# Optimization experiments

Measured on AMD Instinct MI355X. Metric: run time of the kernel, lower is better.

## Reference

```python
import jax, jax.numpy as jnp
import numpy as np

N, D, W, S = 16384, 256, 64, 8  # utterances, embed dim, attention half-window, speakers


def setup_inputs() -> dict:
    key = jax.random.key(0)
    ks = jax.random.split(key, 8)
    scale = 1.0 / np.sqrt(D)
    return {
        "x": jax.random.normal(ks[0], (N, D), jnp.float32),
        "speaker_ids": jax.random.randint(ks[1], (N,), 0, S, jnp.int32),
        "W_att": jax.random.normal(ks[2], (D, D), jnp.float32) * scale,
        "W_pred": jax.random.normal(ks[3], (D, D), jnp.float32) * scale,
        "W_suc": jax.random.normal(ks[4], (D, D), jnp.float32) * scale,
        "W_same": jax.random.normal(ks[5], (D, D), jnp.float32) * scale,
        "W_diff": jax.random.normal(ks[6], (D, D), jnp.float32) * scale,
    }


def reference(x, speaker_ids, W_att, W_pred, W_suc, W_same, W_diff):
    n = x.shape[0]
    pad = jnp.zeros((W, D), x.dtype)
    # windowed gather: for utterance i, neighbors at offsets [-W, W-1] (2W slots)
    win_idx = jnp.arange(n)[:, None] + jnp.arange(2 * W)[None, :]  # index into padded [N+2W]
    xp = jnp.concatenate([pad, x, pad], axis=0)                    # [N+2W, D]
    windows = xp[win_idx]                                          # [N, 2W, D]
    # raw_attn[i,w] = (edge_att_weights(windows[i,w])) . x[i]
    raw_attn = jnp.einsum("nwd,ed,ne->nw", windows, W_att, x)      # [N, 2W]
    attn = jax.nn.softmax(raw_attn, axis=1)
    # relation masks over the band: j = i + offset
    offs = jnp.arange(2 * W) - W                                   # [-W, W-1]
    j = jnp.arange(n)[:, None] + offs[None, :]                     # [N, 2W]
    valid = (j >= 0) & (j < n)
    jc = jnp.clip(j, 0, n - 1)
    same_spk = speaker_ids[jc] == speaker_ids[:, None]
    masks = [
        valid & (offs >= 0)[None, :],   # pred: edges to current/future within window
        valid & (offs < 0)[None, :],    # suc: edges to past within window
        valid & same_spk,               # same speaker within window
        valid & ~same_spk,              # different speaker within window
    ]
    # relation-specific GCN aggregation: h = sum_r A_r @ (x @ W_r), A_r banded
    h = jnp.zeros_like(x)
    for Wr, m in zip([W_pred, W_suc, W_same, W_diff], masks):
        support = x @ Wr                                           # [N, D]
        sp = jnp.concatenate([pad, support, pad], axis=0)[win_idx]  # [N, 2W, D]
        h = h + jnp.einsum("nw,nwd->nd", attn * m, sp)
    return jax.nn.log_softmax(h, axis=1)
```

## Files before the change

kernel.cpp:

```cpp
#include <hip/hip_runtime.h>
#include <hip/hip_bf16.h>

typedef unsigned short u16;
typedef unsigned int u32;
typedef __attribute__((ext_vector_type(8))) short short8;
typedef __attribute__((ext_vector_type(4))) float floatx4;

#define NU 16384
#define DIM 256
#define AMS 208

#define XHo 0u
#define XLo 4194304u
#define XRo 8388608u
#define YHo 12582912u
#define YLo 16777216u
#define ST0 20971520u
#define STROW 16512u
#define STMAT 4227072u
#define WH0o 33652736u
#define WL0o 33718272u
#define WRo  33783808u

__device__ __forceinline__ u16 bfh(float v) {
  return (u16)(__float_as_uint(v) >> 16);
}
__device__ __forceinline__ float bup(u16 u) {
  return __uint_as_float(((u32)u) << 16);
}
__device__ __forceinline__ u16 bfrn(float v) {
  u32 u = __float_as_uint(v);
  return (u16)((u + 0x7fffu + ((u >> 16) & 1u)) >> 16);
}

__global__ __launch_bounds__(256) void xprep(const float* __restrict__ x,
                                             u16* __restrict__ ws) {
  int idx = (blockIdx.x * 256 + threadIdx.x) * 8;
  float4 v0 = *(const float4*)(x + idx);
  float4 v1 = *(const float4*)(x + idx + 4);
  float a[8] = {v0.x, v0.y, v0.z, v0.w, v1.x, v1.y, v1.z, v1.w};
  u16 h[8], l[8], r[8];
#pragma unroll
  for (int q = 0; q < 8; ++q) {
    h[q] = bfh(a[q]);
    l[q] = bfh(a[q] - bup(h[q]));
    r[q] = bfrn(a[q]);
  }
  *(uint4*)(ws + XHo + idx) = *(const uint4*)h;
  *(uint4*)(ws + XLo + idx) = *(const uint4*)l;
  *(uint4*)(ws + XRo + idx) = *(const uint4*)r;
}

__global__ __launch_bounds__(256) void wpgz(
    const float* __restrict__ wat, const float* __restrict__ wpr,
    const float* __restrict__ wsu, const float* __restrict__ wsm,
    const float* __restrict__ wdf, u16* __restrict__ ws) {
  const int b = blockIdx.x, t = threadIdx.x;
  if (b < 32) {
    const int s = b & 7, mat = b >> 3, n = t;
    const float* Wa = (mat == 0) ? wat : (mat == 1) ? wpr : (mat == 2) ? wsm : wsu;
    const float* Wb = (mat == 0) ? wat : (mat == 1) ? wsu : (mat == 2) ? wdf : wdf;
    const float c1  = (mat == 0) ? 0.f : (mat == 3) ? 1.f : -1.f;
    u16 hbuf[32], lbuf[32];
#pragma unroll 8
    for (int k = 0; k < 32; ++k) {
      float v = Wa[(s * 32 + k) * 256 + n] + c1 * Wb[(s * 32 + k) * 256 + n];
      if (mat == 0) { hbuf[k] = bfh(v); lbuf[k] = bfh(v - bup(hbuf[k])); }
      else          { hbuf[k] = bfrn(v); }
    }
    u16* dh = ws + ((mat == 0) ? WH0o : (WRo + (size_t)(mat - 1) * 65536))
               + (size_t)s * 8192 + n * 32;
#pragma unroll
    for (int p = 0; p < 4; ++p) *(uint4*)(dh + p * 8) = ((const uint4*)hbuf)[p];
    if (mat == 0) {
      u16* dl = ws + WL0o + (size_t)s * 8192 + n * 32;
#pragma unroll
      for (int p = 0; p < 4; ++p) *(uint4*)(dl + p * 8) = ((const uint4*)lbuf)[p];
    }
  } else {
    int g = (b - 32) * 256 + t;
    int r = g >> 13, rem = g & 8191;
    int d = rem >> 5, p = rem & 31;
    size_t base = ST0 + (size_t)r * STMAT + (size_t)d * STROW;
    size_t off = (p < 16) ? (base + p * 4) : (base + 16448 + (p - 16) * 4);
    *(ushort4*)(ws + off) = make_ushort4(0, 0, 0, 0);
  }
}

__global__ __launch_bounds__(512) void gemmS(u16* __restrict__ ws) {
  __shared__ __align__(16) u16 U[37888];

  const int t = threadIdx.x, path = blockIdx.y, row0 = blockIdx.x * 64;
  const int w = t >> 6, ln = t & 15, quad = (t & 63) >> 4, q8 = quad * 8;
  const int n0 = w * 32;

  if (path == 0) {
#pragma unroll
    for (int cc = 0; cc < 8; ++cc) {
      int idx = t + 512 * cc;
      int buf = idx >> 11, e = idx & 2047;
      int row = e >> 5, c8 = (e & 31) * 8;
      *(uint4*)(U + buf * 16896 + row * 264 + c8) =
          *(const uint4*)(ws + (buf ? XLo : XHo) + (size_t)(row0 + row) * 256 + c8);
    }
    __syncthreads();

    floatx4 acc[4][2];
#pragma unroll
    for (int m = 0; m < 4; ++m)
#pragma unroll
      for (int nt = 0; nt < 2; ++nt) acc[m][nt] = (floatx4){0.f, 0.f, 0.f, 0.f};

    for (int s = 0; s < 8; ++s) {
      short8 ah[4], al[4];
#pragma unroll
      for (int m = 0; m < 4; ++m) {
        ah[m] = *(const short8*)(U + (m * 16 + ln) * 264 + s * 32 + q8);
        al[m] = *(const short8*)(U + 16896 + (m * 16 + ln) * 264 + s * 32 + q8);
      }
      short8 bh[2], bl[2];
#pragma unroll
      for (int nt = 0; nt < 2; ++nt) {
        size_t off = (size_t)s * 8192 + (n0 + nt * 16 + ln) * 32 + q8;
        bh[nt] = *(const short8*)(ws + WH0o + off);
        bl[nt] = *(const short8*)(ws + WL0o + off);
      }
#pragma unroll
      for (int m = 0; m < 4; ++m)
#pragma unroll
        for (int nt = 0; nt < 2; ++nt) {
          acc[m][nt] = __builtin_amdgcn_mfma_f32_16x16x32_bf16(ah[m], bh[nt], acc[m][nt], 0, 0, 0);
          acc[m][nt] = __builtin_amdgcn_mfma_f32_16x16x32_bf16(ah[m], bl[nt], acc[m][nt], 0, 0, 0);
          acc[m][nt] = __builtin_amdgcn_mfma_f32_16x16x32_bf16(al[m], bh[nt], acc[m][nt], 0, 0, 0);
        }
    }
#pragma unroll
    for (int m = 0; m < 4; ++m)
#pragma unroll
      for (int nt = 0; nt < 2; ++nt) {
        int col = n0 + nt * 16 + ln;
#pragma unroll
        for (int r = 0; r < 4; ++r) {
          int row = row0 + m * 16 + quad * 4 + r;
          float y = acc[m][nt][r];
          u16 hh = bfh(y);
          ws[YHo + (size_t)row * 256 + col] = hh;
          ws[YLo + (size_t)row * 256 + col] = bfh(y - bup(hh));
        }
      }
  } else {
#pragma unroll
    for (int cc = 0; cc < 4; ++cc) {
      int idx = t + 512 * cc;
      int row = idx >> 5, c8 = (idx & 31) * 8;
      *(uint4*)(U + row * 264 + c8) =
          *(const uint4*)(ws + XRo + (size_t)(row0 + row) * 256 + c8);
    }
    __syncthreads();

    for (int mat = 0; mat < 3; ++mat) {
      floatx4 acc[4][2];
#pragma unroll
      for (int m = 0; m < 4; ++m)
#pragma unroll
        for (int nt = 0; nt < 2; ++nt) acc[m][nt] = (floatx4){0.f, 0.f, 0.f, 0.f};
      for (int s = 0; s < 8; ++s) {
        short8 ah[4];
#pragma unroll
        for (int m = 0; m < 4; ++m)
          ah[m] = *(const short8*)(U + (m * 16 + ln) * 264 + s * 32 + q8);
        short8 bh[2];
#pragma unroll
        for (int nt = 0; nt < 2; ++nt)
          bh[nt] = *(const short8*)(ws + WRo + (size_t)mat * 65536
                                    + (size_t)s * 8192 + (n0 + nt * 16 + ln) * 32 + q8);
#pragma unroll
        for (int m = 0; m < 4; ++m)
#pragma unroll
          for (int nt = 0; nt < 2; ++nt)
            acc[m][nt] = __builtin_amdgcn_mfma_f32_16x16x32_bf16(ah[m], bh[nt], acc[m][nt], 0, 0, 0);
      }
      __syncthreads();
#pragma unroll
      for (int m = 0; m < 4; ++m)
#pragma unroll
        for (int nt = 0; nt < 2; ++nt) {
          int col = n0 + nt * 16 + ln;
          ushort4 pk = make_ushort4(bfrn(acc[m][nt][0]), bfrn(acc[m][nt][1]),
                                    bfrn(acc[m][nt][2]), bfrn(acc[m][nt][3]));
          *(ushort4*)(U + 16896 + col * 80 + m * 16 + quad * 4) = pk;
        }
      __syncthreads();
      u16* STm = ws + ST0 + (size_t)mat * STMAT;
#pragma unroll
      for (int cc = 0; cc < 4; ++cc) {
        int c = t + 512 * cc;
        int d = c >> 3, part = c & 7;
        *(uint4*)(STm + (size_t)d * STROW + 64 + row0 + part * 8) =
            *(const uint4*)(U + 16896 + d * 80 + part * 8);
      }
    }
  }
}

__global__ __launch_bounds__(512) void fused_attn(
    const u16* __restrict__ ws, const int* __restrict__ spk,
    float* __restrict__ out)
{
  __shared__ __align__(16) u16 stg[12288];
  __shared__ __align__(16) u16 Am[64 * AMS];
  __shared__ int spkw[192];
  __shared__ float prt[64][2], prs[64][2];
  __shared__ float red[64][8];

  const int t    = threadIdx.x;
  const int w    = t >> 6;
  const int ln   = t & 15;
  const int quad = (t & 63) >> 4;
  const int q8   = quad * 8;
  const int i0   = blockIdx.x * 64;
  const int mw   = w & 3;
  const int half = w >> 2;

  if (t < 192) spkw[t] = spk[min(max(i0 - 64 + t, 0), NU - 1)];

  floatx4 accP[6];
#pragma unroll
  for (int cc = 0; cc < 6; ++cc) accP[cc] = (floatx4){0.f, 0.f, 0.f, 0.f};

  for (int kd = 0; kd < DIM; kd += 32) {
#pragma unroll
    for (int cc = 0; cc < 3; ++cc) {
      int idx = t + 512 * cc;
      int buf = (idx >= 768) ? 1 : 0;
      int e   = idx - buf * 768;
      int row = e >> 2, c8 = (e & 3) * 8;
      int jc  = min(max(i0 + row - 64, 0), NU - 1);
      *(uint4*)(stg + buf * 6144 + row * 32 + c8) =
          *(const uint4*)(ws + (buf ? XLo : XHo) + (size_t)jc * 256 + kd + c8);
    }
    __syncthreads();

    size_t yo = (size_t)(i0 + mw * 16 + ln) * 256 + kd + q8;
    short8 yh8 = *(const short8*)(ws + YHo + yo);
    short8 yl8 = *(const short8*)(ws + YLo + yo);
#pragma unroll
    for (int cc = 0; cc < 6; ++cc) {
      int xrow = half * 96 + cc * 16 + ln;
      short8 xbh = *(const short8*)(stg + xrow * 32 + q8);
      short8 xbl = *(const short8*)(stg + 6144 + xrow * 32 + q8);
      accP[cc] = __builtin_amdgcn_mfma_f32_16x16x32_bf16(yh8, xbh, accP[cc], 0, 0, 0);
      accP[cc] = __builtin_amdgcn_mfma_f32_16x16x32_bf16(yh8, xbl, accP[cc], 0, 0, 0);
      accP[cc] = __builtin_amdgcn_mfma_f32_16x16x32_bf16(yl8, xbh, accP[cc], 0, 0, 0);
    }
    __syncthreads();
  }

  int  c_of[6];
  bool vj[6];
#pragma unroll
  for (int cc = 0; cc < 6; ++cc) {
    c_of[cc] = half * 96 + cc * 16 + ln;
    int j = i0 + c_of[cc] - 64;
    vj[cc] = (j >= 0) && (j < NU);
  }
#pragma unroll
  for (int r = 0; r < 4; ++r) {
    int row = mw * 16 + quad * 4 + r;
    float mx = -3.4e38f;
#pragma unroll
    for (int cc = 0; cc < 6; ++cc) {
      int rel = c_of[cc] - row;
      bool inb = (rel >= 0) && (rel < 128);
      if (inb) mx = fmaxf(mx, vj[cc] ? accP[cc][r] : 0.f);
    }
#pragma unroll
    for (int o = 1; o < 16; o <<= 1) mx = fmaxf(mx, __shfl_xor(mx, o));
    if (ln == 0) prt[row][half] = mx;
  }
  __syncthreads();
#pragma unroll
  for (int r = 0; r < 4; ++r) {
    int row = mw * 16 + quad * 4 + r;
    float gm = fmaxf(prt[row][0], prt[row][1]);
    float s = 0.f;
#pragma unroll
    for (int cc = 0; cc < 6; ++cc) {
      int rel = c_of[cc] - row;
      bool inb = (rel >= 0) && (rel < 128);
      float vv = vj[cc] ? accP[cc][r] : 0.f;
      float e  = inb ? __expf(vv - gm) : 0.f;
      s += e;
      accP[cc][r] = (inb && vj[cc]) ? e : 0.f;
    }
#pragma unroll
    for (int o = 1; o < 16; o <<= 1) s += __shfl_xor(s, o);
    if (ln == 0) prs[row][half] = s;
  }
  __syncthreads();
#pragma unroll
  for (int r = 0; r < 4; ++r) {
    int row = mw * 16 + quad * 4 + r;
    float inv = 1.f / (prs[row][0] + prs[row][1]);
#pragma unroll
    for (int cc = 0; cc < 6; ++cc)
      Am[row * AMS + c_of[cc]] = bfrn(accP[cc][r] * inv);
  }
  __syncthreads();

  const int n0 = w * 32;
  floatx4 acc2[4][2];
#pragma unroll
  for (int m = 0; m < 4; ++m)
#pragma unroll
    for (int nt = 0; nt < 2; ++nt) acc2[m][nt] = (floatx4){0.f, 0.f, 0.f, 0.f};

  const int arow = t >> 3, aseg = t & 7;
  const int sr = spkw[arow + 64];

  for (int kj = 0; kj < 192; kj += 32) {
    {
      u16 b0[4], b1[4], b2[4];
#pragma unroll
      for (int q = 0; q < 4; ++q) {
        int c = kj + aseg * 4 + q;
        u16 a = Am[arow * AMS + c];
        b0[q] = (c - arow >= 64) ? a : (u16)0;
        b1[q] = (spkw[c] == sr) ? a : (u16)0;
        b2[q] = a;
      }
      *(ushort4*)(stg + (0 * 64 + arow) * 32 + aseg * 4) = *(const ushort4*)b0;
      *(ushort4*)(stg + (2048 + arow * 32) + aseg * 4)   = *(const ushort4*)b1;
      *(ushort4*)(stg + (4096 + arow * 32) + aseg * 4)   = *(const ushort4*)b2;
    }
    __syncthreads();

#pragma unroll
    for (int rel = 0; rel < 3; ++rel) {
      short8 af[4];
#pragma unroll
      for (int m = 0; m < 4; ++m)
        af[m] = *(const short8*)(stg + rel * 2048 + (m * 16 + ln) * 32 + q8);
#pragma unroll
      for (int nt = 0; nt < 2; ++nt) {
        size_t so = (size_t)ST0 + (size_t)rel * STMAT
                  + (size_t)(n0 + nt * 16 + ln) * STROW + (i0 + kj) + q8;
        short8 bf8 = *(const short8*)(ws + so);
#pragma unroll
        for (int m = 0; m < 4; ++m)
          acc2[m][nt] = __builtin_amdgcn_mfma_f32_16x16x32_bf16(af[m], bf8, acc2[m][nt], 0, 0, 0);
      }
    }
    __syncthreads();
  }

#pragma unroll
  for (int m = 0; m < 4; ++m)
#pragma unroll
    for (int r = 0; r < 4; ++r) {
      float v = fmaxf(acc2[m][0][r], acc2[m][1][r]);
#pragma unroll
      for (int o = 1; o < 16; o <<= 1) v = fmaxf(v, __shfl_xor(v, o));
      if (ln == 0) red[m * 16 + quad * 4 + r][w] = v;
    }
  __syncthreads();
  float gmx[4][4];
#pragma unroll
  for (int m = 0; m < 4; ++m)
#pragma unroll
    for (int r = 0; r < 4; ++r) {
      int row = m * 16 + quad * 4 + r;
      float g = red[row][0];
#pragma unroll
      for (int ww = 1; ww < 8; ++ww) g = fmaxf(g, red[row][ww]);
      gmx[m][r] = g;
    }
  __syncthreads();
#pragma unroll
  for (int m = 0; m < 4; ++m)
#pragma unroll
    for (int r = 0; r < 4; ++r) {
      float e = __expf(acc2[m][0][r] - gmx[m][r]) + __expf(acc2[m][1][r] - gmx[m][r]);
#pragma unroll
      for (int o = 1; o < 16; o <<= 1) e += __shfl_xor(e, o);
      if (ln == 0) red[m * 16 + quad * 4 + r][w] = e;
    }
  __syncthreads();
#pragma unroll
  for (int m = 0; m < 4; ++m)
#pragma unroll
    for (int r = 0; r < 4; ++r) {
      int row = m * 16 + quad * 4 + r;
      float s = red[row][0];
#pragma unroll
      for (int ww = 1; ww < 8; ++ww) s += red[row][ww];
      float lse = gmx[m][r] + logf(s);
      size_t rowg = (size_t)(i0 + row) * DIM;
      out[rowg + n0 + ln]      = acc2[m][0][r] - lse;
      out[rowg + n0 + 16 + ln] = acc2[m][1][r] - lse;
    }
}

extern "C" void kernel_launch(void* const* d_in, const int* in_sizes, int n_in,
                              void* d_out, int out_size, void* d_ws, size_t ws_size,
                              hipStream_t stream) {
  const float* x   = (const float*)d_in[0];
  const int*   spk = (const int*)d_in[1];
  const float* wat = (const float*)d_in[2];
  const float* wpr = (const float*)d_in[3];
  const float* wsu = (const float*)d_in[4];
  const float* wsm = (const float*)d_in[5];
  const float* wdf = (const float*)d_in[6];
  float* out = (float*)d_out;
  u16* ws = (u16*)d_ws;

  hipLaunchKernelGGL(xprep, dim3(2048), dim3(256), 0, stream, x, ws);
  hipLaunchKernelGGL(wpgz, dim3(128), dim3(256), 0, stream,
                     wat, wpr, wsu, wsm, wdf, ws);
  hipLaunchKernelGGL(gemmS, dim3(256, 2), dim3(512), 0, stream, ws);
  hipLaunchKernelGGL(fused_attn, dim3(256), dim3(512), 0, stream, ws, spk, out);
}
```

Measured before the change: 156.2 us.

## Fuse all four kernels into one cooperative kernel with grid syncs

```diff
diff --git a/kernel.cpp b/kernel.cpp
--- a/kernel.cpp
+++ b/kernel.cpp
@@ -1,5 +1,8 @@
 #include <hip/hip_runtime.h>
 #include <hip/hip_bf16.h>
+#include <hip/hip_cooperative_groups.h>
+
+namespace cg = cooperative_groups;
 
 typedef unsigned short u16;
 typedef unsigned int u32;
@@ -9,22 +12,18 @@
 #define NU 16384
 #define DIM 256
 #define AMS 208
+#define XST 264
+#define CTS 84
 
 #define XHo 0u
 #define XLo 4194304u
-#define XRo 8388608u
-#define YHo 12582912u
-#define YLo 16777216u
-#define ST0 20971520u
+#define ST0 8388608u
 #define STROW 16512u
 #define STMAT 4227072u
-#define WH0o 33652736u
-#define WL0o 33718272u
-#define WRo  33783808u
-
-__device__ __forceinline__ u16 bfh(float v) {
-  return (u16)(__float_as_uint(v) >> 16);
-}
+#define WH0o 21069824u
+#define WL0o 21135360u
+#define WRo  21200896u
+
 __device__ __forceinline__ float bup(u16 u) {
   return __uint_as_float(((u32)u) << 16);
 }
@@ -33,31 +32,59 @@
   return (u16)((u + 0x7fffu + ((u >> 16) & 1u)) >> 16);
 }
 
-__global__ __launch_bounds__(256) void xprep(const float* __restrict__ x,
-                                             u16* __restrict__ ws) {
-  int idx = (blockIdx.x * 256 + threadIdx.x) * 8;
-  float4 v0 = *(const float4*)(x + idx);
-  float4 v1 = *(const float4*)(x + idx + 4);
-  float a[8] = {v0.x, v0.y, v0.z, v0.w, v1.x, v1.y, v1.z, v1.w};
-  u16 h[8], l[8], r[8];
-#pragma unroll
-  for (int q = 0; q < 8; ++q) {
-    h[q] = bfh(a[q]);
-    l[q] = bfh(a[q] - bup(h[q]));
-    r[q] = bfrn(a[q]);
-  }
-  *(uint4*)(ws + XHo + idx) = *(const uint4*)h;
-  *(uint4*)(ws + XLo + idx) = *(const uint4*)l;
-  *(uint4*)(ws + XRo + idx) = *(const uint4*)r;
-}
-
-__global__ __launch_bounds__(256) void wpgz(
+__global__ __launch_bounds__(512, 2) void fused_all(
+    const float* __restrict__ x, const int* __restrict__ spk,
     const float* __restrict__ wat, const float* __restrict__ wpr,
     const float* __restrict__ wsu, const float* __restrict__ wsm,
-    const float* __restrict__ wdf, u16* __restrict__ ws) {
-  const int b = blockIdx.x, t = threadIdx.x;
-  if (b < 32) {
-    const int s = b & 7, mat = b >> 3, n = t;
+    const float* __restrict__ wdf,
+    float* __restrict__ out, u16* __restrict__ ws)
+{
+  __shared__ __align__(16) u16 A_[2 * 64 * XST];
+  __shared__ __align__(16) u16 B_[256 * CTS];
+  __shared__ __align__(16) u16 Am[64 * AMS];
+  __shared__ int spkw[192];
+  __shared__ float prt[64][2], prs[64][2];
+  __shared__ float red[64][8];
+
+  const int t    = threadIdx.x;
+  const int b    = blockIdx.x;
+  const int w    = t >> 6;
+  const int ln   = t & 15;
+  const int quad = (t & 63) >> 4;
+  const int q8   = quad * 8;
+  const int row0 = b * 64;
+  const int i0   = row0;
+
+  cg::grid_group grid = cg::this_grid();
+
+  if (t < 192) spkw[t] = spk[min(max(i0 - 64 + t, 0), NU - 1)];
+
+#pragma unroll
+  for (int cc = 0; cc < 4; ++cc) {
+    int e = t * 8 + cc * 4096;
+    int row = e >> 8, col = e & 255;
+    const float* xp = x + (size_t)(row0 + row) * DIM + col;
+    float4 v0 = *(const float4*)(xp);
+    float4 v1 = *(const float4*)(xp + 4);
+    float a[8] = {v0.x, v0.y, v0.z, v0.w, v1.x, v1.y, v1.z, v1.w};
+    u16 h[8], l[8];
+#pragma unroll
+    for (int q = 0; q < 8; ++q) {
+      h[q] = bfrn(a[q]);
+      l[q] = bfrn(a[q] - bup(h[q]));
+    }
+    size_t go = (size_t)(row0 + row) * DIM + col;
+    *(uint4*)(ws + XHo + go) = *(const uint4*)h;
+    *(uint4*)(ws + XHo + go + 4) = *(const uint4*)(h + 4);
+    *(uint4*)(ws + XLo + go) = *(const uint4*)l;
+    *(uint4*)(ws + XLo + go + 4) = *(const uint4*)(l + 4);
+    *(uint4*)(A_ + row * XST + col)     = *(const uint4*)h;
+    *(uint4*)(A_ + 64 * XST + row * XST + col) = *(const uint4*)l;
+  }
+  if (b < 16) {
+    const int mat = b >> 2;
+    const int s = (b & 3) * 2 + (t >> 8);
+    const int n = t & 255;
     const float* Wa = (mat == 0) ? wat : (mat == 1) ? wpr : (mat == 2) ? wsm : wsu;
     const float* Wb = (mat == 0) ? wat : (mat == 1) ? wsu : (mat == 2) ? wdf : wdf;
     const float c1  = (mat == 0) ? 0.f : (mat == 3) ? 1.f : -1.f;
@@ -65,8 +92,8 @@
 #pragma unroll 8
     for (int k = 0; k < 32; ++k) {
       float v = Wa[(s * 32 + k) * 256 + n] + c1 * Wb[(s * 32 + k) * 256 + n];
-      if (mat == 0) { hbuf[k] = bfh(v); lbuf[k] = bfh(v - bup(hbuf[k])); }
-      else          { hbuf[k] = bfrn(v); }
+      hbuf[k] = bfrn(v);
+      if (mat == 0) lbuf[k] = bfrn(v - bup(hbuf[k]));
     }
     u16* dh = ws + ((mat == 0) ? WH0o : (WRo + (size_t)(mat - 1) * 65536))
                + (size_t)s * 8192 + n * 32;
@@ -77,152 +104,106 @@
 #pragma unroll
       for (int p = 0; p < 4; ++p) *(uint4*)(dl + p * 8) = ((const uint4*)lbuf)[p];
     }
-  } else {
-    int g = (b - 32) * 256 + t;
+  }
+  if (b >= 32 && b < 80) {
+    int g = (b - 32) * 512 + t;
     int r = g >> 13, rem = g & 8191;
     int d = rem >> 5, p = rem & 31;
     size_t base = ST0 + (size_t)r * STMAT + (size_t)d * STROW;
     size_t off = (p < 16) ? (base + p * 4) : (base + 16448 + (p - 16) * 4);
     *(ushort4*)(ws + off) = make_ushort4(0, 0, 0, 0);
   }
-}
-
-__global__ __launch_bounds__(512) void gemmS(u16* __restrict__ ws) {
-  __shared__ __align__(16) u16 U[37888];
-
-  const int t = threadIdx.x, path = blockIdx.y, row0 = blockIdx.x * 64;
-  const int w = t >> 6, ln = t & 15, quad = (t & 63) >> 4, q8 = quad * 8;
-  const int n0 = w * 32;
-
-  if (path == 0) {
-#pragma unroll
-    for (int cc = 0; cc < 8; ++cc) {
-      int idx = t + 512 * cc;
-      int buf = idx >> 11, e = idx & 2047;
-      int row = e >> 5, c8 = (e & 31) * 8;
-      *(uint4*)(U + buf * 16896 + row * 264 + c8) =
-          *(const uint4*)(ws + (buf ? XLo : XHo) + (size_t)(row0 + row) * 256 + c8);
-    }
-    __syncthreads();
-
-    floatx4 acc[4][2];
-#pragma unroll
-    for (int m = 0; m < 4; ++m)
-#pragma unroll
-      for (int nt = 0; nt < 2; ++nt) acc[m][nt] = (floatx4){0.f, 0.f, 0.f, 0.f};
-
+  __threadfence();
+  grid.sync();
+
+  const int mg = (w & 1) * 2;
+  const int ng = (w >> 1) * 4;
+
+  for (int mat = 0; mat < 3; ++mat) {
+    floatx4 acc[2][4];
+#pragma unroll
+    for (int mi = 0; mi < 2; ++mi)
+#pragma unroll
+      for (int nf = 0; nf < 4; ++nf) acc[mi][nf] = (floatx4){0.f, 0.f, 0.f, 0.f};
     for (int s = 0; s < 8; ++s) {
-      short8 ah[4], al[4];
-#pragma unroll
-      for (int m = 0; m < 4; ++m) {
-        ah[m] = *(const short8*)(U + (m * 16 + ln) * 264 + s * 32 + q8);
-        al[m] = *(const short8*)(U + 16896 + (m * 16 + ln) * 264 + s * 32 + q8);
-      }
-      short8 bh[2], bl[2];
-#pragma unroll
-      for (int nt = 0; nt < 2; ++nt) {
-        size_t off = (size_t)s * 8192 + (n0 + nt * 16 + ln) * 32 + q8;
-        bh[nt] = *(const short8*)(ws + WH0o + off);
-        bl[nt] = *(const short8*)(ws + WL0o + off);
-      }
-#pragma unroll
-      for (int m = 0; m < 4; ++m)
-#pragma unroll
-        for (int nt = 0; nt < 2; ++nt) {
-          acc[m][nt] = __builtin_amdgcn_mfma_f32_16x16x32_bf16(ah[m], bh[nt], acc[m][nt], 0, 0, 0);
-          acc[m][nt] = __builtin_amdgcn_mfma_f32_16x16x32_bf16(ah[m], bl[nt], acc[m][nt], 0, 0, 0);
-          acc[m][nt] = __builtin_amdgcn_mfma_f32_16x16x32_bf16(al[m], bh[nt], acc[m][nt], 0, 0, 0);
+      short8 a0 = *(const short8*)(A_ + ((mg + 0) * 16 + ln) * XST + s * 32 + q8);
+      short8 a1 = *(const short8*)(A_ + ((mg + 1) * 16 + ln) * XST + s * 32 + q8);
+#pragma unroll
+      for (int nf = 0; nf < 4; ++nf) {
+        short8 bh = *(const short8*)(ws + WRo + (size_t)mat * 65536
+                     + (size_t)s * 8192 + ((ng + nf) * 16 + ln) * 32 + q8);
+        acc[0][nf] = __builtin_amdgcn_mfma_f32_16x16x32_bf16(a0, bh, acc[0][nf], 0, 0, 0);
+        acc[1][nf] = __builtin_amdgcn_mfma_f32_16x16x32_bf16(a1, bh, acc[1][nf], 0, 0, 0);
+      }
+    }
+    __syncthreads();
+#pragma unroll
+    for (int mi = 0; mi < 2; ++mi)
+#pragma unroll
+      for (int nf = 0; nf < 4; ++nf) {
+        int col = (ng + nf) * 16 + ln;
+        ushort4 pk = make_ushort4(bfrn(acc[mi][nf][0]), bfrn(acc[mi][nf][1]),
+                                  bfrn(acc[mi][nf][2]), bfrn(acc[mi][nf][3]));
+        *(ushort4*)(B_ + col * CTS + (mg + mi) * 16 + quad * 4) = pk;
+      }
+    __syncthreads();
+    u16* STm = ws + ST0 + (size_t)mat * STMAT;
+#pragma unroll
+    for (int cc = 0; cc < 4; ++cc) {
+      int c = t + 512 * cc;
+      int d = c >> 3, part = c & 7;
+      *(uint4*)(STm + (size_t)d * STROW + 64 + row0 + part * 8) =
+          *(const uint4*)(B_ + d * CTS + part * 8);
+    }
+  }
+
+  {
+    floatx4 acc[2][4];
+#pragma unroll
+    for (int mi = 0; mi < 2; ++mi)
+#pragma unroll
+      for (int nf = 0; nf < 4; ++nf) acc[mi][nf] = (floatx4){0.f, 0.f, 0.f, 0.f};
+    for (int s = 0; s < 8; ++s) {
+      short8 ah[2], al[2];
+#pragma unroll
+      for (int mi = 0; mi < 2; ++mi) {
+        ah[mi] = *(const short8*)(A_ + ((mg + mi) * 16 + ln) * XST + s * 32 + q8);
+        al[mi] = *(const short8*)(A_ + 64 * XST + ((mg + mi) * 16 + ln) * XST + s * 32 + q8);
+      }
+#pragma unroll
+      for (int nf = 0; nf < 4; ++nf) {
+        size_t off = (size_t)s * 8192 + ((ng + nf) * 16 + ln) * 32 + q8;
+        short8 bh = *(const short8*)(ws + WH0o + off);
+        short8 bl = *(const short8*)(ws + WL0o + off);
+#pragma unroll
+        for (int mi = 0; mi < 2; ++mi) {
+          acc[mi][nf] = __builtin_amdgcn_mfma_f32_16x16x32_bf16(ah[mi], bh, acc[mi][nf], 0, 0, 0);
+          acc[mi][nf] = __builtin_amdgcn_mfma_f32_16x16x32_bf16(ah[mi], bl, acc[mi][nf], 0, 0, 0);
+          acc[mi][nf] = __builtin_amdgcn_mfma_f32_16x16x32_bf16(al[mi], bh, acc[mi][nf], 0, 0, 0);
         }
-    }
-#pragma unroll
-    for (int m = 0; m < 4; ++m)
-#pragma unroll
-      for (int nt = 0; nt < 2; ++nt) {
-        int col = n0 + nt * 16 + ln;
+      }
+    }
+    __syncthreads();
+#pragma unroll
+    for (int mi = 0; mi < 2; ++mi)
+#pragma unroll
+      for (int nf = 0; nf < 4; ++nf) {
+        int col = (ng + nf) * 16 + ln;
 #pragma unroll
         for (int r = 0; r < 4; ++r) {
-          int row = row0 + m * 16 + quad * 4 + r;
-          float y = acc[m][nt][r];
-          u16 hh = bfh(y);
-          ws[YHo + (size_t)row * 256 + col] = hh;
-          ws[YLo + (size_t)row * 256 + col] = bfh(y - bup(hh));
+          int row = (mg + mi) * 16 + quad * 4 + r;
+          float y = acc[mi][nf][r];
+          u16 hh = bfrn(y);
+          A_[row * XST + col] = hh;
+          A_[64 * XST + row * XST + col] = bfrn(y - bup(hh));
         }
       }
-  } else {
-#pragma unroll
-    for (int cc = 0; cc < 4; ++cc) {
-      int idx = t + 512 * cc;
-      int row = idx >> 5, c8 = (idx & 31) * 8;
-      *(uint4*)(U + row * 264 + c8) =
-          *(const uint4*)(ws + XRo + (size_t)(row0 + row) * 256 + c8);
-    }
-    __syncthreads();
-
-    for (int mat = 0; mat < 3; ++mat) {
-      floatx4 acc[4][2];
-#pragma unroll
-      for (int m = 0; m < 4; ++m)
-#pragma unroll
-        for (int nt = 0; nt < 2; ++nt) acc[m][nt] = (floatx4){0.f, 0.f, 0.f, 0.f};
-      for (int s = 0; s < 8; ++s) {
-        short8 ah[4];
-#pragma unroll
-        for (int m = 0; m < 4; ++m)
-          ah[m] = *(const short8*)(U + (m * 16 + ln) * 264 + s * 32 + q8);
-        short8 bh[2];
-#pragma unroll
-        for (int nt = 0; nt < 2; ++nt)
-          bh[nt] = *(const short8*)(ws + WRo + (size_t)mat * 65536
-                                    + (size_t)s * 8192 + (n0 + nt * 16 + ln) * 32 + q8);
-#pragma unroll
-        for (int m = 0; m < 4; ++m)
-#pragma unroll
-          for (int nt = 0; nt < 2; ++nt)
-            acc[m][nt] = __builtin_amdgcn_mfma_f32_16x16x32_bf16(ah[m], bh[nt], acc[m][nt], 0, 0, 0);
-      }
-      __syncthreads();
-#pragma unroll
-      for (int m = 0; m < 4; ++m)
-#pragma unroll
-        for (int nt = 0; nt < 2; ++nt) {
-          int col = n0 + nt * 16 + ln;
-          ushort4 pk = make_ushort4(bfrn(acc[m][nt][0]), bfrn(acc[m][nt][1]),
-                                    bfrn(acc[m][nt][2]), bfrn(acc[m][nt][3]));
-          *(ushort4*)(U + 16896 + col * 80 + m * 16 + quad * 4) = pk;
-        }
-      __syncthreads();
-      u16* STm = ws + ST0 + (size_t)mat * STMAT;
-#pragma unroll
-      for (int cc = 0; cc < 4; ++cc) {
-        int c = t + 512 * cc;
-        int d = c >> 3, part = c & 7;
-        *(uint4*)(STm + (size_t)d * STROW + 64 + row0 + part * 8) =
-            *(const uint4*)(U + 16896 + d * 80 + part * 8);
-      }
-    }
-  }
-}
-
-__global__ __launch_bounds__(512) void fused_attn(
-    const u16* __restrict__ ws, const int* __restrict__ spk,
-    float* __restrict__ out)
-{
-  __shared__ __align__(16) u16 stg[12288];
-  __shared__ __align__(16) u16 Am[64 * AMS];
-  __shared__ int spkw[192];
-  __shared__ float prt[64][2], prs[64][2];
-  __shared__ float red[64][8];
-
-  const int t    = threadIdx.x;
-  const int w    = t >> 6;
-  const int ln   = t & 15;
-  const int quad = (t & 63) >> 4;
-  const int q8   = quad * 8;
-  const int i0   = blockIdx.x * 64;
+  }
+  __threadfence();
+  grid.sync();
+
   const int mw   = w & 3;
   const int half = w >> 2;
-
-  if (t < 192) spkw[t] = spk[min(max(i0 - 64 + t, 0), NU - 1)];
 
   floatx4 accP[6];
 #pragma unroll
@@ -236,19 +217,18 @@
       int e   = idx - buf * 768;
       int row = e >> 2, c8 = (e & 3) * 8;
       int jc  = min(max(i0 + row - 64, 0), NU - 1);
-      *(uint4*)(stg + buf * 6144 + row * 32 + c8) =
+      *(uint4*)(B_ + buf * 6144 + row * 32 + c8) =
           *(const uint4*)(ws + (buf ? XLo : XHo) + (size_t)jc * 256 + kd + c8);
     }
     __syncthreads();
 
-    size_t yo = (size_t)(i0 + mw * 16 + ln) * 256 + kd + q8;
-    short8 yh8 = *(const short8*)(ws + YHo + yo);
-    short8 yl8 = *(const short8*)(ws + YLo + yo);
+    short8 yh8 = *(const short8*)(A_ + (mw * 16 + ln) * XST + kd + q8);
+    short8 yl8 = *(const short8*)(A_ + 64 * XST + (mw * 16 + ln) * XST + kd + q8);
 #pragma unroll
     for (int cc = 0; cc < 6; ++cc) {
       int xrow = half * 96 + cc * 16 + ln;
-      short8 xbh = *(const short8*)(stg + xrow * 32 + q8);
-      short8 xbl = *(const short8*)(stg + 6144 + xrow * 32 + q8);
+      short8 xbh = *(const short8*)(B_ + xrow * 32 + q8);
+      short8 xbl = *(const short8*)(B_ + 6144 + xrow * 32 + q8);
       accP[cc] = __builtin_amdgcn_mfma_f32_16x16x32_bf16(yh8, xbh, accP[cc], 0, 0, 0);
       accP[cc] = __builtin_amdgcn_mfma_f32_16x16x32_bf16(yh8, xbl, accP[cc], 0, 0, 0);
       accP[cc] = __builtin_amdgcn_mfma_f32_16x16x32_bf16(yl8, xbh, accP[cc], 0, 0, 0);
@@ -329,9 +309,9 @@
         b1[q] = (spkw[c] == sr) ? a : (u16)0;
         b2[q] = a;
       }
-      *(ushort4*)(stg + (0 * 64 + arow) * 32 + aseg * 4) = *(const ushort4*)b0;
-      *(ushort4*)(stg + (2048 + arow * 32) + aseg * 4)   = *(const ushort4*)b1;
-      *(ushort4*)(stg + (4096 + arow * 32) + aseg * 4)   = *(const ushort4*)b2;
+      *(ushort4*)(B_ + (0 * 64 + arow) * 32 + aseg * 4) = *(const ushort4*)b0;
+      *(ushort4*)(B_ + (2048 + arow * 32) + aseg * 4)   = *(const ushort4*)b1;
+      *(ushort4*)(B_ + (4096 + arow * 32) + aseg * 4)   = *(const ushort4*)b2;
     }
     __syncthreads();
 
@@ -340,7 +320,7 @@
       short8 af[4];
 #pragma unroll
       for (int m = 0; m < 4; ++m)
-        af[m] = *(const short8*)(stg + rel * 2048 + (m * 16 + ln) * 32 + q8);
+        af[m] = *(const short8*)(B_ + rel * 2048 + (m * 16 + ln) * 32 + q8);
 #pragma unroll
       for (int nt = 0; nt < 2; ++nt) {
         size_t so = (size_t)ST0 + (size_t)rel * STMAT
@@ -414,9 +394,8 @@
   float* out = (float*)d_out;
   u16* ws = (u16*)d_ws;
 
-  hipLaunchKernelGGL(xprep, dim3(2048), dim3(256), 0, stream, x, ws);
-  hipLaunchKernelGGL(wpgz, dim3(128), dim3(256), 0, stream,
-                     wat, wpr, wsu, wsm, wdf, ws);
-  hipLaunchKernelGGL(gemmS, dim3(256, 2), dim3(512), 0, stream, ws);
-  hipLaunchKernelGGL(fused_attn, dim3(256), dim3(512), 0, stream, ws, spk, out);
+  void* args[] = {(void*)&x, (void*)&spk, (void*)&wat, (void*)&wpr,
+                  (void*)&wsu, (void*)&wsm, (void*)&wdf, (void*)&out, (void*)&ws};
+  hipLaunchCooperativeKernel((const void*)fused_all, dim3(256), dim3(512),
+                             args, 0, stream);
 }
```

Result: slower. 323.9 us (+107.4%).
